# Kernel tuning notes

Hardware: AMD Instinct MI355X
Metric: run time of the kernel (lower is better)

The kernel has to match this reference:

```python
import jax, jax.numpy as jnp
import numpy as np

B, S, D, NH, HFF, VOCAB = 128, 100, 512, 8, 2048, 50000
DH = D // NH
GH, GL, NC = 256, 2, 10  # GRU hidden, GRU layers, num classes
NE = 3  # num encoders


def setup_inputs() -> dict:
    key = jax.random.key(0)
    ks = jax.random.split(key, 32)
    f = lambda k, shp, s=0.02: (jax.random.normal(k, shp, dtype=jnp.float32) * s)
    inp = {
        'x': jax.random.randint(ks[0], (B, S), 0, VOCAB),
        'x1': jnp.ones((B, S), dtype=jnp.float32),
        'emb': f(ks[1], (VOCAB, D)),
        'Wq': f(ks[2], (NE, D, D)), 'bq': jnp.zeros((NE, D)),
        'Wk': f(ks[3], (NE, D, D)), 'bk': jnp.zeros((NE, D)),
        'Wv': f(ks[4], (NE, D, D)), 'bv': jnp.zeros((NE, D)),
        'Wo': f(ks[5], (NE, D, D)), 'bo': jnp.zeros((NE, D)),
        'g1': jnp.ones((NE, D)), 'be1': jnp.zeros((NE, D)),
        'W1': f(ks[6], (NE, D, HFF)), 'b1': jnp.zeros((NE, HFF)),
        'W2': f(ks[7], (NE, HFF, D)), 'b2': jnp.zeros((NE, D)),
        'g2': jnp.ones((NE, D)), 'be2': jnp.zeros((NE, D)),
        'gru_Wih': f(ks[8], (GL, 2, 3 * GH, D)),
        'gru_Whh': f(ks[9], (GL, 2, 3 * GH, GH)),
        'gru_bih': jnp.zeros((GL, 2, 3 * GH)),
        'gru_bhh': jnp.zeros((GL, 2, 3 * GH)),
        'fc_W': f(ks[10], (2 * GH + D, NC)), 'fc_b': jnp.zeros((NC,)),
    }
    return inp


def _layer_norm(x, g, b, eps=1e-5):
    m = jnp.mean(x, axis=-1, keepdims=True)
    v = jnp.mean((x - m) ** 2, axis=-1, keepdims=True)
    return (x - m) / jnp.sqrt(v + eps) * g + b


def _forward(x, emb, Wq, bq, Wk, bk, Wv, bv, Wo, bo, g1, be1, W1, b1, W2, b2,
             g2, be2, gru_Wih, gru_Whh, gru_bih, gru_bhh, fc_W, fc_b):
    out = emb[x]  # [B, S, D]
    scale = DH ** -0.5
    for l in range(NE):
        # NOTE: torch code uses a contiguous view(B*NH, -1, DH), not a
        # transpose-based head split; plain reshape reproduces it exactly.
        Q = (out @ Wq[l] + bq[l]).reshape(B * NH, S, DH)
        K = (out @ Wk[l] + bk[l]).reshape(B * NH, S, DH)
        V = (out @ Wv[l] + bv[l]).reshape(B * NH, S, DH)
        att = jax.nn.softmax(jnp.einsum('bqd,bkd->bqk', Q, K) * scale, axis=-1)
        ctx = (att @ V).reshape(B, S, D)
        out = _layer_norm(ctx @ Wo[l] + bo[l] + out, g1[l], be1[l])
        ff = jnp.maximum(out @ W1[l] + b1[l], 0.0) @ W2[l] + b2[l]
        out = _layer_norm(ff + out, g2[l], be2[l])
    embed_feat = out

    # Bidirectional multi-layer GRU (torch cuDNN formulation), seq-major.
    h_seq = jnp.transpose(out, (1, 0, 2))  # [S, B, D]
    for l in range(GL):
        dirs = []
        for d in range(2):
            Wih, Whh = gru_Wih[l, d], gru_Whh[l, d]
            bih, bhh = gru_bih[l, d], gru_bhh[l, d]
            xp = h_seq @ Wih.T + bih  # [S, B, 3H]

            def step(h, xpt, Whh=Whh, bhh=bhh):
                hp = h @ Whh.T + bhh
                r = jax.nn.sigmoid(xpt[:, :GH] + hp[:, :GH])
                z = jax.nn.sigmoid(xpt[:, GH:2 * GH] + hp[:, GH:2 * GH])
                n = jnp.tanh(xpt[:, 2 * GH:] + r * hp[:, 2 * GH:])
                hn = (1.0 - z) * n + z * h
                return hn, hn

            h0 = jnp.zeros((B, GH), dtype=h_seq.dtype)
            _, ys = jax.lax.scan(step, h0, xp, reverse=(d == 1))
            dirs.append(ys)
        h_seq = jnp.concatenate(dirs, axis=-1)  # [S, B, 2H]
    gru_out = jnp.transpose(h_seq, (1, 0, 2))  # [B, S, 2H]

    feat = jnp.maximum(jnp.concatenate([embed_feat, gru_out], axis=-1), 0.0)
    pooled = jnp.max(feat, axis=1)  # MaxPool1d(pad_size) over seq -> [B, 2H+D]
    return pooled @ fc_W + fc_b


def reference(x, x1, emb, Wq, bq, Wk, bk, Wv, bv, Wo, bo, g1, be1, W1, b1,
              W2, b2, g2, be2, gru_Wih, gru_Whh, gru_bih, gru_bhh, fc_W, fc_b):
    # x1 (mask) is dead in the original module: the masked attention result is
    # immediately overwritten by the unmasked call, so it does not affect output.
    return _forward(x, emb, Wq, bq, Wk, bk, Wv, bv, Wo, bo, g1, be1, W1, b1,
                    W2, b2, g2, be2, gru_Wih, gru_Whh, gru_bih, gru_bhh,
                    fc_W, fc_b)
```

## Files before the change

kernel.cpp:

```cpp
#include <hip/hip_runtime.h>
#include <cstdint>

typedef __bf16 bf16x8 __attribute__((ext_vector_type(8)));
typedef float f32x4 __attribute__((ext_vector_type(4)));
typedef unsigned short ushort8 __attribute__((ext_vector_type(8)));

#define DEV __device__ __forceinline__
#define MFMA16(a, b, c) __builtin_amdgcn_mfma_f32_16x16x32_bf16((a), (b), (c), 0, 0, 0)
#define MFMA_AG(acc, hf, wf) \
  asm("v_mfma_f32_16x16x32_bf16 %0, %1, %2, %0" : "+v"(acc) : "v"(hf), "a"(wf))

DEV unsigned short f2b(float x) {
  union { float f; unsigned int u; } c; c.f = x;
  unsigned int u = c.u + 0x7fffu + ((c.u >> 16) & 1u);
  return (unsigned short)(u >> 16);
}
DEV float b2f(unsigned short x) {
  union { unsigned int u; float f; } c; c.u = ((unsigned int)x) << 16;
  return c.f;
}
DEV void gld_lds16(const void* g, void* l) {
  __builtin_amdgcn_global_load_lds(
      (const __attribute__((address_space(1))) unsigned int*)(uintptr_t)g,
      (__attribute__((address_space(3))) unsigned int*)(uintptr_t)l, 16, 0, 0);
}

__global__ __launch_bounds__(256) void convT_k(const float* __restrict__ in,
                                               unsigned short* __restrict__ out,
                                               int K, int N) {
  __shared__ float tile[64][65];
  int k0 = blockIdx.x * 64, n0 = blockIdx.y * 64;
  int wv = threadIdx.x >> 6, ln = threadIdx.x & 63;
  #pragma unroll
  for (int i = 0; i < 16; ++i) {
    int r = wv * 16 + i;
    tile[r][ln] = in[(size_t)(k0 + r) * N + (n0 + ln)];
  }
  __syncthreads();
  #pragma unroll
  for (int i = 0; i < 16; ++i) {
    int r = wv * 16 + i;
    out[(size_t)(n0 + r) * K + (k0 + ln)] = f2b(tile[ln][r]);
  }
}

__global__ void convB_k(const float* __restrict__ in, unsigned short* __restrict__ out, int n) {
  int stride = gridDim.x * blockDim.x;
  for (int i = blockIdx.x * blockDim.x + threadIdx.x; i < n; i += stride)
    out[i] = f2b(in[i]);
}

__global__ __launch_bounds__(256) void biasC_k(const float* __restrict__ bih,
                                               const float* __restrict__ bhh,
                                               float* __restrict__ cb) {
  int i = blockIdx.x * 256 + threadIdx.x;
  if (i < 4 * 768) {
    int c = i % 768;
    cb[i] = bih[i] + (c < 512 ? bhh[i] : 0.f);
  }
}

__global__ __launch_bounds__(256) void embed_k(const int* __restrict__ x, const float* __restrict__ emb,
                                               float* __restrict__ cf, unsigned short* __restrict__ cb) {
  int row = blockIdx.x * 4 + (threadIdx.x >> 6);
  int lane = threadIdx.x & 63;
  int tok = x[row];
  const float4* src = (const float4*)(emb + (size_t)tok * 512 + lane * 8);
  float4 a = src[0], b = src[1];
  float4* dst = (float4*)(cf + (size_t)row * 512 + lane * 8);
  dst[0] = a; dst[1] = b;
  ushort8 pk;
  pk[0] = f2b(a.x); pk[1] = f2b(a.y); pk[2] = f2b(a.z); pk[3] = f2b(a.w);
  pk[4] = f2b(b.x); pk[5] = f2b(b.y); pk[6] = f2b(b.z); pk[7] = f2b(b.w);
  *(ushort8*)(cb + (size_t)row * 512 + lane * 8) = pk;
}

DEV void stage_tile(const unsigned short* g, int ld, unsigned short* lds, int lane, int wave) {
  #pragma unroll
  for (int i = 0; i < 2; ++i) {
    int r0 = (i * 4 + wave) * 16;
    const unsigned short* src = g + (size_t)(r0 + (lane >> 2)) * ld + (lane & 3) * 8;
    gld_lds16(src, lds + r0 * 32);
  }
}

template <int RELU, int RES, int OF32, int OB16>
__global__ __launch_bounds__(256) void gemm_k(
    const unsigned short* __restrict__ A, const unsigned short* __restrict__ BT,
    const float* __restrict__ bias, const float* __restrict__ res,
    float* __restrict__ Cf, unsigned short* __restrict__ Cb,
    int M, int N, int K) {
  __shared__ unsigned short sA[2][128 * 32];
  __shared__ unsigned short sB[2][128 * 32];
  int tid = threadIdx.x, lane = tid & 63, wave = tid >> 6;
  int m0 = blockIdx.x * 128, n0 = blockIdx.y * 128;
  int lm = lane & 15, lk = (lane >> 4) * 8;
  int wr = wave >> 1, wc = wave & 1;
  f32x4 acc[4][4];
  #pragma unroll
  for (int i = 0; i < 4; ++i)
    #pragma unroll
    for (int j = 0; j < 4; ++j) acc[i][j] = (f32x4){0.f, 0.f, 0.f, 0.f};
  const unsigned short* Ab = A + (size_t)m0 * K;
  const unsigned short* Bb = BT + (size_t)n0 * K;
  int nk = K >> 5;
  stage_tile(Ab, K, sA[0], lane, wave);
  stage_tile(Bb, K, sB[0], lane, wave);
  __syncthreads();
  int buf = 0;
  for (int t = 0; t < nk; ++t) {
    if (t + 1 < nk) {
      stage_tile(Ab + (t + 1) * 32, K, sA[buf ^ 1], lane, wave);
      stage_tile(Bb + (t + 1) * 32, K, sB[buf ^ 1], lane, wave);
    }
    bf16x8 aF[4], bF[4];
    #pragma unroll
    for (int i = 0; i < 4; ++i) aF[i] = *(const bf16x8*)&sA[buf][(wr * 64 + i * 16 + lm) * 32 + lk];
    #pragma unroll
    for (int j = 0; j < 4; ++j) bF[j] = *(const bf16x8*)&sB[buf][(wc * 64 + j * 16 + lm) * 32 + lk];
    #pragma unroll
    for (int i = 0; i < 4; ++i)
      #pragma unroll
      for (int j = 0; j < 4; ++j) acc[i][j] = MFMA16(aF[i], bF[j], acc[i][j]);
    __syncthreads();
    buf ^= 1;
  }
  #pragma unroll
  for (int i = 0; i < 4; ++i) {
    int gr0 = m0 + wr * 64 + i * 16 + (lane >> 4) * 4;
    #pragma unroll
    for (int j = 0; j < 4; ++j) {
      int gc = n0 + wc * 64 + j * 16 + lm;
      float bv = bias[gc];
      #pragma unroll
      for (int q = 0; q < 4; ++q) {
        size_t idx = (size_t)(gr0 + q) * N + gc;
        float v = acc[i][j][q] + bv;
        if (RES) v += res[idx];
        if (RELU) v = fmaxf(v, 0.f);
        if (OF32) Cf[idx] = v;
        if (OB16) Cb[idx] = f2b(v);
      }
    }
  }
}

__global__ __launch_bounds__(256) void attn_k(const unsigned short* __restrict__ Q,
                                              const unsigned short* __restrict__ Kv,
                                              const unsigned short* __restrict__ V,
                                              unsigned short* __restrict__ ctx) {
  __shared__ unsigned short Ks[112 * 64];
  __shared__ unsigned short VT[64 * 128];
  __shared__ unsigned short Ps[112 * 128];
  int g = blockIdx.x;
  size_t base = (size_t)g * 6400;
  int tid = threadIdx.x, lane = tid & 63, wave = tid >> 6;
  int lm = lane & 15, lg = lane >> 4, lk = lg * 8;
  for (int idx = tid; idx < 112 * 8; idx += 256) {
    int row = idx >> 3, c8 = (idx & 7) * 8;
    int rr = row < 100 ? row : 99;
    *(ushort8*)&Ks[row * 64 + c8] = *(const ushort8*)&Kv[base + (size_t)rr * 64 + c8];
  }
  for (int idx = tid; idx < 64 * 28; idx += 256) { int c = idx / 28, j = idx % 28; VT[c * 128 + 100 + j] = 0; }
  for (int idx = tid; idx < 112 * 16; idx += 256) { int r = idx / 16, c = idx % 16; Ps[r * 128 + 112 + c] = 0; }
  for (int idx = tid; idx < 6400; idx += 256) {
    int c = idx / 100, j = idx % 100;
    VT[c * 128 + j] = V[base + (size_t)j * 64 + c];
  }
  __syncthreads();
  for (int rt = wave; rt < 7; rt += 4) {
    int arow = rt * 16 + lm;
    int qrow = arow < 100 ? arow : 99;
    bf16x8 aF0 = *(const bf16x8*)&Q[base + (size_t)qrow * 64 + lk];
    bf16x8 aF1 = *(const bf16x8*)&Q[base + (size_t)qrow * 64 + 32 + lk];
    f32x4 sc[7];
    #pragma unroll
    for (int ct = 0; ct < 7; ++ct) {
      bf16x8 b0 = *(const bf16x8*)&Ks[(ct * 16 + lm) * 64 + lk];
      bf16x8 b1 = *(const bf16x8*)&Ks[(ct * 16 + lm) * 64 + 32 + lk];
      f32x4 a = {0.f, 0.f, 0.f, 0.f};
      a = MFMA16(aF0, b0, a);
      a = MFMA16(aF1, b1, a);
      sc[ct] = a;
    }
    #pragma unroll
    for (int q = 0; q < 4; ++q) {
      float mx = -1e30f;
      #pragma unroll
      for (int ct = 0; ct < 7; ++ct) {
        int col = ct * 16 + lm;
        float v = sc[ct][q] * 0.125f;
        if (col < 100) mx = fmaxf(mx, v);
      }
      for (int off = 1; off < 16; off <<= 1) mx = fmaxf(mx, __shfl_xor(mx, off));
      float sum = 0.f; float pv[7];
      #pragma unroll
      for (int ct = 0; ct < 7; ++ct) {
        int col = ct * 16 + lm;
        float e = (col < 100) ? __expf(sc[ct][q] * 0.125f - mx) : 0.f;
        pv[ct] = e; sum += e;
      }
      for (int off = 1; off < 16; off <<= 1) sum += __shfl_xor(sum, off);
      float inv = 1.f / sum;
      int prow = rt * 16 + lg * 4 + q;
      #pragma unroll
      for (int ct = 0; ct < 7; ++ct) Ps[prow * 128 + ct * 16 + lm] = f2b(pv[ct] * inv);
    }
  }
  __syncthreads();
  for (int rt = wave; rt < 7; rt += 4) {
    bf16x8 aP[4];
    #pragma unroll
    for (int kc = 0; kc < 4; ++kc) aP[kc] = *(const bf16x8*)&Ps[(rt * 16 + lm) * 128 + kc * 32 + lk];
    #pragma unroll
    for (int ctp = 0; ctp < 4; ++ctp) {
      f32x4 o = {0.f, 0.f, 0.f, 0.f};
      #pragma unroll
      for (int kc = 0; kc < 4; ++kc) {
        bf16x8 bV = *(const bf16x8*)&VT[(ctp * 16 + lm) * 128 + kc * 32 + lk];
        o = MFMA16(aP[kc], bV, o);
      }
      #pragma unroll
      for (int q = 0; q < 4; ++q) {
        int ri = rt * 16 + lg * 4 + q;
        if (ri < 100) ctx[base + (size_t)ri * 64 + ctp * 16 + lm] = f2b(o[q]);
      }
    }
  }
}

__global__ __launch_bounds__(256) void ln_k(const float* __restrict__ in, const float* __restrict__ gamma,
                                            const float* __restrict__ beta, float* __restrict__ outF,
                                            unsigned short* __restrict__ outB) {
  int row = blockIdx.x * 4 + (threadIdx.x >> 6);
  int lane = threadIdx.x & 63;
  const float* p = in + (size_t)row * 512 + lane * 8;
  float4 v0 = *(const float4*)p;
  float4 v1 = *(const float4*)(p + 4);
  float x[8] = {v0.x, v0.y, v0.z, v0.w, v1.x, v1.y, v1.z, v1.w};
  float s = 0.f;
  #pragma unroll
  for (int e = 0; e < 8; ++e) s += x[e];
  #pragma unroll
  for (int off = 1; off < 64; off <<= 1) s += __shfl_xor(s, off);
  float mean = s * (1.f / 512.f);
  float vs = 0.f;
  #pragma unroll
  for (int e = 0; e < 8; ++e) { float d = x[e] - mean; vs += d * d; }
  #pragma unroll
  for (int off = 1; off < 64; off <<= 1) vs += __shfl_xor(vs, off);
  float rstd = rsqrtf(vs * (1.f / 512.f) + 1e-5f);
  int c0 = lane * 8;
  ushort8 pk;
  #pragma unroll
  for (int e = 0; e < 8; ++e) {
    float y = (x[e] - mean) * rstd * gamma[c0 + e] + beta[c0 + e];
    x[e] = y; pk[e] = f2b(y);
  }
  float4* po = (float4*)(outF + (size_t)row * 512 + c0);
  po[0] = make_float4(x[0], x[1], x[2], x[3]);
  po[1] = make_float4(x[4], x[5], x[6], x[7]);
  *(ushort8*)(outB + (size_t)row * 512 + c0) = pk;
}

__global__ __launch_bounds__(128) void seqT_k(const unsigned short* __restrict__ in,
                                              unsigned short* __restrict__ out) {
  int o = blockIdx.x;
  int s = o >> 7, b = o & 127;
  const uint2* src = (const uint2*)(in + (size_t)(b * 100 + s) * 512);
  uint2* dst = (uint2*)(out + (size_t)o * 512);
  dst[threadIdx.x] = src[threadIdx.x];
}

__global__ __launch_bounds__(512) __attribute__((amdgpu_waves_per_eu(2, 2))) void gru_k(
    const unsigned short* __restrict__ WhhB,
    const float* __restrict__ bhh,
    const float* __restrict__ xp,
    unsigned short* __restrict__ hout)
{
  __shared__ unsigned short hb[2][16 * 256];
  __shared__ char ldsn[131072];
  const int dir = blockIdx.x >> 3, bsl = blockIdx.x & 7;
  const int tid = threadIdx.x, lane = tid & 63, w = tid >> 6;
  const int lm = lane & 15, lg = lane >> 4, lk = lg * 8;
  const int col = w * 32 + lm * 2;

  for (int i = tid; i < 16 * 256; i += 512) hb[0][i] = 0;

  {
    const unsigned short* wn = WhhB + (size_t)(dir * 768 + 512) * 256;
    #pragma unroll
    for (int ct = 0; ct < 2; ++ct)
      #pragma unroll
      for (int kt = 0; kt < 8; ++kt) {
        const unsigned short* src = wn + (size_t)(col + ct) * 256 + kt * 32 + lk;
        gld_lds16(src, ldsn + (size_t)w * 16384 + (ct * 8 + kt) * 1024);
      }
  }

  bf16x8 wr[2][8], wz[2][8];
  #pragma unroll
  for (int ct = 0; ct < 2; ++ct) {
    const unsigned short* wpr = WhhB + (size_t)(dir * 768 + col + ct) * 256;
    const unsigned short* wpz = WhhB + (size_t)(dir * 768 + 256 + col + ct) * 256;
    #pragma unroll
    for (int kt = 0; kt < 8; ++kt) {
      wr[ct][kt] = *(const bf16x8*)&wpr[kt * 32 + lk];
      wz[ct][kt] = *(const bf16x8*)&wpz[kt * 32 + lk];
    }
  }
  #pragma unroll
  for (int ct = 0; ct < 2; ++ct)
    #pragma unroll
    for (int kt = 0; kt < 8; ++kt) {
      asm("" : "+a"(wr[ct][kt]));
      asm("" : "+a"(wz[ct][kt]));
    }

  float bh2[2];
  bh2[0] = bhh[dir * 768 + 512 + col];
  bh2[1] = bhh[dir * 768 + 512 + col + 1];
  float hprev[2][4] = {{0.f, 0.f, 0.f, 0.f}, {0.f, 0.f, 0.f, 0.f}};

  const int s0 = dir ? 99 : 0, sstep = dir ? -1 : 1;
  unsigned short* hob = hout + ((size_t)(s0 * 128 + bsl * 16 + lg * 4)) * 512 + dir * 256 + col;
  const ptrdiff_t hstep = (ptrdiff_t)sstep * 65536;
  const float* xpb = xp + ((size_t)dir * 100 + s0) * 98304 + (size_t)(bsl * 16 + lg * 4) * 768 + col;
  const ptrdiff_t xstep = (ptrdiff_t)sstep * 98304;

  __syncthreads();

  const int swz = (lm & 7) << 4;
  const char* nb = ldsn + (size_t)w * 16384 + lane * 16;
  for (int t = 0; t < 100; ++t) {
    const int cur = t & 1;
    float2 xv[3][4];
    #pragma unroll
    for (int g = 0; g < 3; ++g)
      #pragma unroll
      for (int q = 0; q < 4; ++q)
        xv[g][q] = *(const float2*)(xpb + q * 768 + g * 256);
    const char* hbase = (const char*)&hb[cur][0] + lm * 512;
    bf16x8 hF[8];
    #pragma unroll
    for (int kt = 0; kt < 8; ++kt)
      hF[kt] = *(const bf16x8*)(hbase + ((kt * 64 + lg * 16) ^ swz));
    f32x4 aR[2], aZ[2], aN[2];
    #pragma unroll
    for (int ct = 0; ct < 2; ++ct) {
      aR[ct] = (f32x4){0.f, 0.f, 0.f, 0.f};
      aZ[ct] = (f32x4){0.f, 0.f, 0.f, 0.f};
      aN[ct] = (f32x4){0.f, 0.f, 0.f, 0.f};
    }
    #pragma unroll
    for (int kt = 0; kt < 8; ++kt) {
      bf16x8 n0 = *(const bf16x8*)(nb + kt * 1024);
      bf16x8 n1 = *(const bf16x8*)(nb + 8192 + kt * 1024);
      MFMA_AG(aR[0], hF[kt], wr[0][kt]);
      MFMA_AG(aZ[0], hF[kt], wz[0][kt]);
      MFMA_AG(aR[1], hF[kt], wr[1][kt]);
      MFMA_AG(aZ[1], hF[kt], wz[1][kt]);
      aN[0] = MFMA16(hF[kt], n0, aN[0]);
      aN[1] = MFMA16(hF[kt], n1, aN[1]);
    }
    #pragma unroll
    for (int q = 0; q < 4; ++q) {
      const int row = lg * 4 + q;
      float hn01[2];
      #pragma unroll
      for (int ct = 0; ct < 2; ++ct) {
        float xr = (ct ? xv[0][q].y : xv[0][q].x);
        float xz = (ct ? xv[1][q].y : xv[1][q].x);
        float xn = (ct ? xv[2][q].y : xv[2][q].x);
        float r = 1.f / (1.f + __expf(-(xr + aR[ct][q])));
        float z = 1.f / (1.f + __expf(-(xz + aZ[ct][q])));
        float nbv = xn + r * (aN[ct][q] + bh2[ct]);
        float n = 1.f - 2.f / (__expf(2.f * nbv) + 1.f);
        float hn = (1.f - z) * n + z * hprev[ct][q];
        hprev[ct][q] = hn;
        hn01[ct] = hn;
      }
      unsigned int pk;
      asm("v_cvt_pk_bf16_f32 %0, %1, %2" : "=v"(pk) : "v"(hn01[0]), "v"(hn01[1]));
      *(unsigned int*)((char*)&hb[cur ^ 1][0] + row * 512 + ((w * 64 + lm * 4) ^ ((row & 7) << 4))) = pk;
      *(unsigned int*)&hob[q * 512] = pk;
    }
    asm volatile("s_waitcnt lgkmcnt(0)" ::: "memory");
    __builtin_amdgcn_s_barrier();
    hob += hstep;
    xpb += xstep;
  }
}

__global__ __launch_bounds__(256) void pool_k(const float* __restrict__ ef, const unsigned short* __restrict__ h2,
                                              float* __restrict__ pooled) {
  int b = blockIdx.x, tid = threadIdx.x;
  for (int c = tid; c < 1024; c += 256) {
    float m = 0.f;
    if (c < 512) {
      for (int s = 0; s < 100; ++s) m = fmaxf(m, ef[((size_t)b * 100 + s) * 512 + c]);
    } else {
      int cc = c - 512;
      for (int s = 0; s < 100; ++s) m = fmaxf(m, b2f(h2[((size_t)s * 128 + b) * 512 + cc]));
    }
    pooled[b * 1024 + c] = m;
  }
}

__global__ __launch_bounds__(64) void fc_k(const float* __restrict__ pooled, const float* __restrict__ W,
                                           const float* __restrict__ bias, float* __restrict__ out) {
  int b = blockIdx.x, lane = threadIdx.x;
  float a[10];
  #pragma unroll
  for (int n = 0; n < 10; ++n) a[n] = 0.f;
  for (int k = lane; k < 1024; k += 64) {
    float pv = pooled[b * 1024 + k];
    const float* wr = W + k * 10;
    #pragma unroll
    for (int n = 0; n < 10; ++n) a[n] += pv * wr[n];
  }
  #pragma unroll
  for (int n = 0; n < 10; ++n)
    for (int off = 32; off > 0; off >>= 1) a[n] += __shfl_xor(a[n], off);
  if (lane == 0) {
    #pragma unroll
    for (int n = 0; n < 10; ++n) out[b * 10 + n] = a[n] + bias[n];
  }
}

extern "C" void kernel_launch(void* const* d_in, const int* in_sizes, int n_in,
                              void* d_out, int out_size, void* d_ws, size_t ws_size,
                              hipStream_t stream) {
  (void)in_sizes; (void)n_in; (void)out_size;
  const int*   x   = (const int*)d_in[0];
  const float* emb = (const float*)d_in[2];
  const float* Wq  = (const float*)d_in[3];  const float* bq  = (const float*)d_in[4];
  const float* Wk  = (const float*)d_in[5];  const float* bk  = (const float*)d_in[6];
  const float* Wv  = (const float*)d_in[7];  const float* bv  = (const float*)d_in[8];
  const float* Wo  = (const float*)d_in[9];  const float* bo  = (const float*)d_in[10];
  const float* g1  = (const float*)d_in[11]; const float* be1 = (const float*)d_in[12];
  const float* W1  = (const float*)d_in[13]; const float* b1  = (const float*)d_in[14];
  const float* W2  = (const float*)d_in[15]; const float* b2  = (const float*)d_in[16];
  const float* g2  = (const float*)d_in[17]; const float* be2 = (const float*)d_in[18];
  const float* Wih = (const float*)d_in[19]; const float* Whh = (const float*)d_in[20];
  const float* bih = (const float*)d_in[21]; const float* bhh = (const float*)d_in[22];
  const float* fcW = (const float*)d_in[23]; const float* fcb = (const float*)d_in[24];

  if (ws_size < 193986560ULL) return;
  char* ws = (char*)d_ws;

  const size_t O_CURF = 0, O_CURBF = 26214400, O_WQT = 39321600, O_WKT = 40894464,
               O_WVT = 42467328, O_WOT = 44040192, O_W1T = 45613056, O_W2T = 51904512,
               O_WIH = 58195968, O_WHH = 61341696, O_A = 62914560;
  float* cur_f = (float*)(ws + O_CURF);
  unsigned short* cur_bf = (unsigned short*)(ws + O_CURBF);
  unsigned short* WqT = (unsigned short*)(ws + O_WQT);
  unsigned short* WkT = (unsigned short*)(ws + O_WKT);
  unsigned short* WvT = (unsigned short*)(ws + O_WVT);
  unsigned short* WoT = (unsigned short*)(ws + O_WOT);
  unsigned short* W1T = (unsigned short*)(ws + O_W1T);
  unsigned short* W2T = (unsigned short*)(ws + O_W2T);
  unsigned short* WihB = (unsigned short*)(ws + O_WIH);
  unsigned short* WhhB = (unsigned short*)(ws + O_WHH);
  float* cbias = (float*)(ws + O_WQT);
  unsigned short* Qb  = (unsigned short*)(ws + O_A);
  unsigned short* Kb  = (unsigned short*)(ws + O_A + 13107200);
  unsigned short* Vb  = (unsigned short*)(ws + O_A + 26214400);
  unsigned short* ctx = (unsigned short*)(ws + O_A + 39321600);
  unsigned short* ff1 = (unsigned short*)(ws + O_A + 52428800);
  float* tmp_f = (float*)(ws + O_A + 104857600);
  unsigned short* xseq  = (unsigned short*)(ws + O_A);
  float* xp             = (float*)(ws + O_A + 13107200);
  unsigned short* hout1 = (unsigned short*)(ws + O_A + 91750400);
  unsigned short* hout2 = (unsigned short*)(ws + O_A + 104857600);
  float* pooled         = (float*)(ws + O_A + 117964800);

  for (int l = 0; l < 3; ++l) {
    convT_k<<<dim3(8, 8), 256, 0, stream>>>(Wq + (size_t)l * 262144, WqT + (size_t)l * 262144, 512, 512);
    convT_k<<<dim3(8, 8), 256, 0, stream>>>(Wk + (size_t)l * 262144, WkT + (size_t)l * 262144, 512, 512);
    convT_k<<<dim3(8, 8), 256, 0, stream>>>(Wv + (size_t)l * 262144, WvT + (size_t)l * 262144, 512, 512);
    convT_k<<<dim3(8, 8), 256, 0, stream>>>(Wo + (size_t)l * 262144, WoT + (size_t)l * 262144, 512, 512);
    convT_k<<<dim3(8, 32), 256, 0, stream>>>(W1 + (size_t)l * 1048576, W1T + (size_t)l * 1048576, 512, 2048);
    convT_k<<<dim3(32, 8), 256, 0, stream>>>(W2 + (size_t)l * 1048576, W2T + (size_t)l * 1048576, 2048, 512);
  }
  convB_k<<<1024, 256, 0, stream>>>(Wih, WihB, 2 * 2 * 768 * 512);
  convB_k<<<512, 256, 0, stream>>>(Whh, WhhB, 2 * 2 * 768 * 256);

  embed_k<<<3200, 256, 0, stream>>>(x, emb, cur_f, cur_bf);

  for (int l = 0; l < 3; ++l) {
    gemm_k<0, 0, 0, 1><<<dim3(100, 4), 256, 0, stream>>>(cur_bf, WqT + (size_t)l * 262144, bq + l * 512, nullptr, nullptr, Qb, 12800, 512, 512);
    gemm_k<0, 0, 0, 1><<<dim3(100, 4), 256, 0, stream>>>(cur_bf, WkT + (size_t)l * 262144, bk + l * 512, nullptr, nullptr, Kb, 12800, 512, 512);
    gemm_k<0, 0, 0, 1><<<dim3(100, 4), 256, 0, stream>>>(cur_bf, WvT + (size_t)l * 262144, bv + l * 512, nullptr, nullptr, Vb, 12800, 512, 512);
    attn_k<<<1024, 256, 0, stream>>>(Qb, Kb, Vb, ctx);
    gemm_k<0, 1, 1, 0><<<dim3(100, 4), 256, 0, stream>>>(ctx, WoT + (size_t)l * 262144, bo + l * 512, cur_f, tmp_f, nullptr, 12800, 512, 512);
    ln_k<<<3200, 256, 0, stream>>>(tmp_f, g1 + l * 512, be1 + l * 512, cur_f, cur_bf);
    gemm_k<1, 0, 0, 1><<<dim3(100, 16), 256, 0, stream>>>(cur_bf, W1T + (size_t)l * 1048576, b1 + l * 2048, nullptr, nullptr, ff1, 12800, 2048, 512);
    gemm_k<0, 1, 1, 0><<<dim3(100, 4), 256, 0, stream>>>(ff1, W2T + (size_t)l * 1048576, b2 + l * 512, cur_f, tmp_f, nullptr, 12800, 512, 2048);
    ln_k<<<3200, 256, 0, stream>>>(tmp_f, g2 + l * 512, be2 + l * 512, cur_f, cur_bf);
  }

  biasC_k<<<12, 256, 0, stream>>>(bih, bhh, cbias);
  seqT_k<<<12800, 128, 0, stream>>>(cur_bf, xseq);
  for (int l = 0; l < 2; ++l) {
    const unsigned short* Ain = (l == 0) ? xseq : hout1;
    for (int d = 0; d < 2; ++d)
      gemm_k<0, 0, 1, 0><<<dim3(100, 6), 256, 0, stream>>>(
          Ain, WihB + ((size_t)l * 2 + d) * 768 * 512, cbias + (l * 2 + d) * 768, nullptr,
          xp + (size_t)d * 9830400, nullptr, 12800, 768, 512);
    gru_k<<<16, 512, 0, stream>>>(WhhB + (size_t)l * 2 * 768 * 256, bhh + l * 2 * 768, xp,
                                  (l == 0) ? hout1 : hout2);
  }

  pool_k<<<128, 256, 0, stream>>>(cur_f, hout2, pooled);
  fc_k<<<128, 64, 0, stream>>>(pooled, fcW, fcb, (float*)d_out);
}
```

Measured before the change: 1.381 ms.

## Split GRU batch across twice the blocks and store input projections in bf16

The recurrent GRU kernel now launches 32 blocks of 8 batch rows each instead of 16 blocks of 16 rows. The MFMA still runs on 16 rows, but only half the lanes do the gate math and stores. This spreads the sequential recurrence over more CUs so each step has less elementwise work. The input-projection GEMM also writes bf16 instead of fp32, halving xp traffic in the per-step loads. The trade-off is wasted MFMA work on padded rows and some precision loss on the gate inputs.

```diff
diff --git a/kernel.cpp b/kernel.cpp
--- a/kernel.cpp
+++ b/kernel.cpp
@@ -17,6 +17,14 @@
 }
 DEV float b2f(unsigned short x) {
   union { unsigned int u; float f; } c; c.u = ((unsigned int)x) << 16;
+  return c.f;
+}
+DEV float bhi(unsigned int pk) {
+  union { unsigned int u; float f; } c; c.u = pk & 0xFFFF0000u;
+  return c.f;
+}
+DEV float blo(unsigned int pk) {
+  union { unsigned int u; float f; } c; c.u = pk << 16;
   return c.f;
 }
 DEV void gld_lds16(const void* g, void* l) {
@@ -275,17 +283,17 @@
 __global__ __launch_bounds__(512) __attribute__((amdgpu_waves_per_eu(2, 2))) void gru_k(
     const unsigned short* __restrict__ WhhB,
     const float* __restrict__ bhh,
-    const float* __restrict__ xp,
+    const unsigned short* __restrict__ xp,
     unsigned short* __restrict__ hout)
 {
   __shared__ unsigned short hb[2][16 * 256];
   __shared__ char ldsn[131072];
-  const int dir = blockIdx.x >> 3, bsl = blockIdx.x & 7;
+  const int dir = blockIdx.x >> 4, bsl = blockIdx.x & 15;
   const int tid = threadIdx.x, lane = tid & 63, w = tid >> 6;
   const int lm = lane & 15, lg = lane >> 4, lk = lg * 8;
   const int col = w * 32 + lm * 2;
 
-  for (int i = tid; i < 16 * 256; i += 512) hb[0][i] = 0;
+  for (int i = tid; i < 2 * 16 * 256; i += 512) hb[0][i] = 0;
 
   {
     const unsigned short* wn = WhhB + (size_t)(dir * 768 + 512) * 256;
@@ -323,9 +331,9 @@
   float hprev[2][4] = {{0.f, 0.f, 0.f, 0.f}, {0.f, 0.f, 0.f, 0.f}};
 
   const int s0 = dir ? 99 : 0, sstep = dir ? -1 : 1;
-  unsigned short* hob = hout + ((size_t)(s0 * 128 + bsl * 16 + lg * 4)) * 512 + dir * 256 + col;
+  unsigned short* hob = hout + ((size_t)(s0 * 128 + bsl * 8 + lg * 4)) * 512 + dir * 256 + col;
   const ptrdiff_t hstep = (ptrdiff_t)sstep * 65536;
-  const float* xpb = xp + ((size_t)dir * 100 + s0) * 98304 + (size_t)(bsl * 16 + lg * 4) * 768 + col;
+  const unsigned short* xpb = xp + ((size_t)dir * 100 + s0) * 98304 + (size_t)(bsl * 8 + lg * 4) * 768 + col;
   const ptrdiff_t xstep = (ptrdiff_t)sstep * 98304;
 
   __syncthreads();
@@ -334,12 +342,14 @@
   const char* nb = ldsn + (size_t)w * 16384 + lane * 16;
   for (int t = 0; t < 100; ++t) {
     const int cur = t & 1;
-    float2 xv[3][4];
-    #pragma unroll
-    for (int g = 0; g < 3; ++g)
-      #pragma unroll
-      for (int q = 0; q < 4; ++q)
-        xv[g][q] = *(const float2*)(xpb + q * 768 + g * 256);
+    unsigned int xv[3][4];
+    if (lg < 2) {
+      #pragma unroll
+      for (int g = 0; g < 3; ++g)
+        #pragma unroll
+        for (int q = 0; q < 4; ++q)
+          xv[g][q] = *(const unsigned int*)(xpb + q * 768 + g * 256);
+    }
     const char* hbase = (const char*)&hb[cur][0] + lm * 512;
     bf16x8 hF[8];
     #pragma unroll
@@ -363,27 +373,29 @@
       aN[0] = MFMA16(hF[kt], n0, aN[0]);
       aN[1] = MFMA16(hF[kt], n1, aN[1]);
     }
-    #pragma unroll
-    for (int q = 0; q < 4; ++q) {
-      const int row = lg * 4 + q;
-      float hn01[2];
-      #pragma unroll
-      for (int ct = 0; ct < 2; ++ct) {
-        float xr = (ct ? xv[0][q].y : xv[0][q].x);
-        float xz = (ct ? xv[1][q].y : xv[1][q].x);
-        float xn = (ct ? xv[2][q].y : xv[2][q].x);
-        float r = 1.f / (1.f + __expf(-(xr + aR[ct][q])));
-        float z = 1.f / (1.f + __expf(-(xz + aZ[ct][q])));
-        float nbv = xn + r * (aN[ct][q] + bh2[ct]);
-        float n = 1.f - 2.f / (__expf(2.f * nbv) + 1.f);
-        float hn = (1.f - z) * n + z * hprev[ct][q];
-        hprev[ct][q] = hn;
-        hn01[ct] = hn;
-      }
-      unsigned int pk;
-      asm("v_cvt_pk_bf16_f32 %0, %1, %2" : "=v"(pk) : "v"(hn01[0]), "v"(hn01[1]));
-      *(unsigned int*)((char*)&hb[cur ^ 1][0] + row * 512 + ((w * 64 + lm * 4) ^ ((row & 7) << 4))) = pk;
-      *(unsigned int*)&hob[q * 512] = pk;
+    if (lg < 2) {
+      #pragma unroll
+      for (int q = 0; q < 4; ++q) {
+        const int row = lg * 4 + q;
+        float hn01[2];
+        #pragma unroll
+        for (int ct = 0; ct < 2; ++ct) {
+          float xr = ct ? bhi(xv[0][q]) : blo(xv[0][q]);
+          float xz = ct ? bhi(xv[1][q]) : blo(xv[1][q]);
+          float xn = ct ? bhi(xv[2][q]) : blo(xv[2][q]);
+          float r = 1.f / (1.f + __expf(-(xr + aR[ct][q])));
+          float z = 1.f / (1.f + __expf(-(xz + aZ[ct][q])));
+          float nbv = xn + r * (aN[ct][q] + bh2[ct]);
+          float n = 1.f - 2.f / (__expf(2.f * nbv) + 1.f);
+          float hn = (1.f - z) * n + z * hprev[ct][q];
+          hprev[ct][q] = hn;
+          hn01[ct] = hn;
+        }
+        unsigned int pk;
+        asm("v_cvt_pk_bf16_f32 %0, %1, %2" : "=v"(pk) : "v"(hn01[0]), "v"(hn01[1]));
+        *(unsigned int*)((char*)&hb[cur ^ 1][0] + row * 512 + ((w * 64 + lm * 4) ^ ((row & 7) << 4))) = pk;
+        *(unsigned int*)&hob[q * 512] = pk;
+      }
     }
     asm volatile("s_waitcnt lgkmcnt(0)" ::: "memory");
     __builtin_amdgcn_s_barrier();
@@ -470,7 +482,7 @@
   unsigned short* ff1 = (unsigned short*)(ws + O_A + 52428800);
   float* tmp_f = (float*)(ws + O_A + 104857600);
   unsigned short* xseq  = (unsigned short*)(ws + O_A);
-  float* xp             = (float*)(ws + O_A + 13107200);
+  unsigned short* xpB   = (unsigned short*)(ws + O_A + 13107200);
   unsigned short* hout1 = (unsigned short*)(ws + O_A + 91750400);
   unsigned short* hout2 = (unsigned short*)(ws + O_A + 104857600);
   float* pooled         = (float*)(ws + O_A + 117964800);
@@ -505,10 +517,10 @@
   for (int l = 0; l < 2; ++l) {
     const unsigned short* Ain = (l == 0) ? xseq : hout1;
     for (int d = 0; d < 2; ++d)
-      gemm_k<0, 0, 1, 0><<<dim3(100, 6), 256, 0, stream>>>(
+      gemm_k<0, 0, 0, 1><<<dim3(100, 6), 256, 0, stream>>>(
           Ain, WihB + ((size_t)l * 2 + d) * 768 * 512, cbias + (l * 2 + d) * 768, nullptr,
-          xp + (size_t)d * 9830400, nullptr, 12800, 768, 512);
-    gru_k<<<16, 512, 0, stream>>>(WhhB + (size_t)l * 2 * 768 * 256, bhh + l * 2 * 768, xp,
+          nullptr, xpB + (size_t)d * 9830400, 12800, 768, 512);
+    gru_k<<<32, 512, 0, stream>>>(WhhB + (size_t)l * 2 * 768 * 256, bhh + l * 2 * 768, xpB,
                                   (l == 0) ? hout1 : hout2);
   }
 
```

Result: no change. 1.385 ms (+0.3%).
